# Performance work log

Hardware: AMD Instinct MI355X
Metric: run time of the kernel (lower is better)

## Reference

```python
import jax, jax.numpy as jnp
import numpy as np

WSZ = 8
HEADS = 8
FILTER_RATE = 0.3
EPS = 1e-5


def layer_norm(x, w, b):
    mu = x.mean(-1, keepdims=True)
    var = ((x - mu) ** 2).mean(-1, keepdims=True)
    return (x - mu) * jax.lax.rsqrt(var + EPS) * w + b


def setup_inputs() -> dict:
    key = jax.random.key(0)
    ks = jax.random.split(key, 8)
    B, C, H, W = 2, 256, 512, 512
    C2 = 2 * C
    s = 0.02
    return {
        "feature_map": jax.random.normal(ks[0], (B, C, H, W), jnp.float32),
        "uncertain_map": jax.random.uniform(ks[1], (B, H, W), jnp.float32),
        "norm_w": jnp.ones((C,), jnp.float32),
        "norm_b": jnp.zeros((C,), jnp.float32),
        "lin0_w": jax.random.normal(ks[2], (C, C2), jnp.float32) * s,
        "lin0_b": jnp.zeros((C2,), jnp.float32),
        "qkv0_w": jax.random.normal(ks[3], (C2, 3 * C2), jnp.float32) * s,
        "lin1_w": jax.random.normal(ks[4], (C2, C2), jnp.float32) * s,
        "lin1_b": jnp.zeros((C2,), jnp.float32),
        "qkv1_w": jax.random.normal(ks[5], (C2, 3 * C2), jnp.float32) * s,
        "proj_w": jax.random.normal(ks[6], (C2, C), jnp.float32) * s,
        "proj_b": jnp.zeros((C,), jnp.float32),
    }


def _window_attn(xf, qkv_w, scale, winsz, C2):
    # xf: (N, winsz, C2)
    qkv = (xf @ qkv_w).reshape(-1, winsz, 3, HEADS, C2 // HEADS)
    q, k, v = qkv[:, :, 0], qkv[:, :, 1], qkv[:, :, 2]  # (N, winsz, H, dh)
    a = jnp.einsum("nqhd,nkhd->nhqk", q, k) * scale
    a = jax.nn.softmax(a, axis=-1)
    o = jnp.einsum("nhqk,nkhd->nqhd", a, v).reshape(-1, winsz, C2)
    return xf + o


def reference(feature_map, uncertain_map, norm_w, norm_b, lin0_w, lin0_b,
              qkv0_w, lin1_w, lin1_b, qkv1_w, proj_w, proj_b):
    B, C, H, W = feature_map.shape
    wsz = WSZ
    nH, nW = H // wsz, W // wsz
    nWin, winsz = nH * nW, wsz * wsz
    nWF = int(nWin * FILTER_RATE)
    C2 = 2 * C
    scale = (C // HEADS) ** -0.5  # module uses C//num_heads, not C2//num_heads

    # window partition
    x = jnp.transpose(feature_map, (0, 2, 3, 1))  # B H W C
    win_x = x.reshape(B, nH, wsz, nW, wsz, C).transpose(0, 1, 3, 2, 4, 5)
    win_x = win_x.reshape(B * nWin, winsz, C)
    win_unc = uncertain_map.reshape(B, nH, wsz, nW, wsz).transpose(0, 1, 3, 2, 4)
    win_unc = win_unc.reshape(B, nWin, winsz)

    # topk window selection by mean uncertainty
    score = win_unc.mean(-1)  # (B, nWin)
    _, idx = jax.lax.top_k(score, nWF)  # (B, nWF)
    flat_idx = (idx + jnp.arange(B)[:, None] * nWin).reshape(-1)  # (B*nWF,)

    xw = win_x[flat_idx]  # gather: (B*nWF, winsz, C)
    xn = layer_norm(xw, norm_w, norm_b)

    # local branch: repeat 0
    xf = jax.nn.gelu(xn @ lin0_w + lin0_b, approximate=False)
    xf = _window_attn(xf, qkv0_w, scale, winsz, C2)
    # repeat 1
    xf = xf + jax.nn.gelu(xf @ lin1_w + lin1_b, approximate=False)
    xf = _window_attn(xf, qkv1_w, scale, winsz, C2)

    out_f = xn + jax.nn.gelu(xf @ proj_w + proj_b, approximate=False)

    # scatter-add back into unnormalized windows
    win_x = win_x.at[flat_idx].add(out_f)

    x = win_x.reshape(B, nH, nW, wsz, wsz, C).transpose(0, 1, 3, 2, 4, 5)
    x = x.reshape(B, H, W, C)
    return jnp.transpose(x, (0, 3, 1, 2))
```

## Files before the change

kernel.cpp:

```cpp
#include <hip/hip_runtime.h>
#include <math.h>

typedef unsigned short u16;
typedef unsigned int   u32;
typedef __attribute__((ext_vector_type(8))) short bf16x8;
typedef __attribute__((ext_vector_type(4))) float f32x4;

#define DEV static __device__ __forceinline__

DEV u16 f2b(float f) {
  union { float f; u32 u; } v; v.f = f;
  u32 r = v.u + 0x7FFFu + ((v.u >> 16) & 1u);
  return (u16)(r >> 16);
}
DEV float b2f(u16 h) {
  union { u32 u; float f; } v; v.u = ((u32)h) << 16;
  return v.f;
}
DEV float gelu_f(float x) { return 0.5f * x * (1.0f + erff(x * 0.70710678118654752f)); }

DEV void gload16(const u16* g, u16* l) {
  __builtin_amdgcn_global_load_lds(
      (const __attribute__((address_space(1))) void*)g,
      (__attribute__((address_space(3))) void*)l, 16, 0, 0);
}

__global__ void k_transpose_w(const float* __restrict__ src, u16* __restrict__ dst,
                              int K, int N) {
  long t = (long)blockIdx.x * 256 + threadIdx.x;
  if (t >= (long)K * N) return;
  int n = (int)(t / K), k = (int)(t % K);
  dst[t] = f2b(src[(long)k * N + n]);
}

__global__ void k_scores(const float* __restrict__ unc, float* __restrict__ scores) {
  int id = blockIdx.x * 256 + threadIdx.x;
  if (id >= 8192) return;
  int b = id >> 12, win = id & 4095;
  int h0 = (win >> 6) << 3, w0 = (win & 63) << 3;
  float r[8] = {0.f,0.f,0.f,0.f,0.f,0.f,0.f,0.f};
  for (int i = 0; i < 8; ++i) {
    long base = ((long)(b * 512 + h0 + i)) * 512 + w0;
    #pragma unroll
    for (int j = 0; j < 8; ++j) r[j] += unc[base + j];
  }
  float s = ((r[0] + r[1]) + (r[2] + r[3])) + ((r[4] + r[5]) + (r[6] + r[7]));
  scores[id] = s * (1.0f / 64.0f);
}

__global__ __launch_bounds__(1024) void k_topk(
    const float* __restrict__ scores, int* __restrict__ row2win,
    int* __restrict__ win2row, int nWF) {
  __shared__ float ls[4096];
  __shared__ int   li[4096];
  const int b = blockIdx.x;
  const int tid = threadIdx.x;
  for (int i = tid; i < 4096; i += 1024) {
    ls[i] = scores[b * 4096 + i];
    li[i] = i;
    win2row[b * 4096 + i] = -1;
  }
  __syncthreads();
  for (int k = 2; k <= 4096; k <<= 1) {
    for (int j = k >> 1; j > 0; j >>= 1) {
      for (int t = tid; t < 2048; t += 1024) {
        int i = ((t / j) * (j << 1)) + (t % j);
        int ixj = i + j;
        bool up = ((i & k) == 0);
        float sa = ls[i], sb = ls[ixj];
        int ia = li[i], ib = li[ixj];
        bool g = (sa > sb) || (sa == sb && ia < ib);
        if (g != up) { ls[i] = sb; ls[ixj] = sa; li[i] = ib; li[ixj] = ia; }
      }
      __syncthreads();
    }
  }
  for (int r = tid; r < nWF; r += 1024) {
    int win = li[r];
    row2win[b * nWF + r] = (b << 12) | win;
    win2row[b * 4096 + win] = b * nWF + r;
  }
}

__global__ __launch_bounds__(256) void k_gather_ln(
    const float* __restrict__ fm, const float* __restrict__ nw,
    const float* __restrict__ nb, const int* __restrict__ row2win,
    u16* __restrict__ xn, int winStart) {
  __shared__ float sx[64 * 256];
  const int tid = threadIdx.x;
  const int rw = row2win[winStart + blockIdx.x];
  const int b = rw >> 12, win = rw & 4095;
  const int h0 = (win >> 6) << 3, w0 = (win & 63) << 3;
  {
    const int c8 = tid >> 3, h = tid & 7;
    #pragma unroll
    for (int cc = 0; cc < 8; ++cc) {
      const int c = cc * 32 + c8;
      long base = ((long)(b * 256 + c) * 512 + h0 + h) * 512 + w0;
      float4 v0 = *(const float4*)(fm + base);
      float4 v1 = *(const float4*)(fm + base + 4);
      float vv[8] = {v0.x, v0.y, v0.z, v0.w, v1.x, v1.y, v1.z, v1.w};
      #pragma unroll
      for (int j = 0; j < 8; ++j) {
        int tok = h * 8 + j;
        sx[tok * 256 + (c ^ ((tok & 15) << 1))] = vv[j];
      }
    }
  }
  __syncthreads();
  const int tok = tid >> 2, g = tid & 3;
  const int swz = (tok & 15) << 1;
  float sum = 0.f;
  for (int q = 0; q < 64; ++q) sum += sx[tok * 256 + ((g * 64 + q) ^ swz)];
  sum += __shfl_xor(sum, 1);
  sum += __shfl_xor(sum, 2);
  const float mu = sum * (1.0f / 256.0f);
  float s2 = 0.f;
  for (int q = 0; q < 64; ++q) {
    float d = sx[tok * 256 + ((g * 64 + q) ^ swz)] - mu;
    s2 += d * d;
  }
  s2 += __shfl_xor(s2, 1);
  s2 += __shfl_xor(s2, 2);
  const float rs = rsqrtf(s2 * (1.0f / 256.0f) + 1e-5f);
  long obase = ((long)blockIdx.x * 64 + tok) * 256 + g * 64;
  for (int q8 = 0; q8 < 8; ++q8) {
    u16 tmp[8];
    #pragma unroll
    for (int e = 0; e < 8; ++e) {
      int c = g * 64 + q8 * 8 + e;
      float v = (sx[tok * 256 + (c ^ swz)] - mu) * rs * nw[c] + nb[c];
      tmp[e] = f2b(v);
    }
    *(ulonglong2*)(xn + obase + q8 * 8) = *(const ulonglong2*)tmp;
  }
}

template <int EPI, int NT, int KD>
__global__ __launch_bounds__(512, 2) void k_gemm256(
    const u16* __restrict__ A, const u16* __restrict__ Bt,
    const float* __restrict__ bias, const u16* __restrict__ Res,
    u16* __restrict__ Y, int N, int nWork) {
  constexpr int NKT = KD / 64;
  constexpr int LG_NKT = (KD == 512) ? 3 : 2;
  constexpr int NIP = KD / 128;
  constexpr int LG_NIP = (KD == 512) ? 2 : 1;
  __shared__ __attribute__((aligned(16))) u16 S[65536];
  const int tid = threadIdx.x;
  const int l = tid & 63, wid = tid >> 6;
  const int wm = wid >> 2, wn = wid & 3;

  const int slot = ((blockIdx.x & 7) << 5) | (blockIdx.x >> 3);
  const int q = nWork >> 8, rr = nWork & 255;
  const int wrkBase = slot * q + (slot < rr ? slot : rr);
  const int myN = q + (slot < rr ? 1 : 0);
  if (myN == 0) return;

  const int srow = wid * 8 + (l >> 3);
  const int k0b = ((l & 7) << 4) ^ ((l >> 3) << 4);
  const int vko = k0b >> 1;
  char* ldsS = (char*)S + wid * 1024 + l * 16;
  const char* Sb = (const char*)S;

  f32x4 acc[8][4] = {};
  bf16x8 bfrag[4][2];
  bf16x8 af[2][2];

#define STG(G, ISB, H) do { \
    const int wig_ = (G) >> LG_NKT; \
    const int ktg_ = (G) & (NKT - 1); \
    const int wrkg_ = wrkBase + wig_; \
    const int tmg_ = wrkg_ / NT, tng_ = wrkg_ % NT; \
    const u16* g_ = (ISB) ? Bt + (long)(tng_ * 256 + srow) * KD + vko \
                          : A + (long)(tmg_ * 256 + srow) * KD + vko; \
    char* lp_ = ldsS + ((G) & 1) * 65536 + (ISB) * 32768 + (H) * 16384; \
    gload16(g_ + (long)((H) * 128) * KD + ktg_ * 64, (u16*)lp_); \
    gload16(g_ + (long)((H) * 128 + 64) * KD + ktg_ * 64, (u16*)(lp_ + 8192)); \
  } while (0)

#define DS_B(T) do { \
    _Pragma("unroll") for (int ni_ = 0; ni_ < 4; ++ni_) { \
      const int r_ = wn * 64 + ni_ * 16 + (l & 15); \
      _Pragma("unroll") for (int kk_ = 0; kk_ < 2; ++kk_) { \
        const int kb_ = kk_ * 64 + ((l >> 4) << 4); \
        bfrag[ni_][kk_] = *(const bf16x8*)(Sb + ((T) & 1) * 65536 + 32768 + r_ * 128 + (kb_ ^ ((r_ & 7) << 4))); \
      } } \
  } while (0)

#define DS_A(T, Q) do { \
    _Pragma("unroll") for (int m2_ = 0; m2_ < 2; ++m2_) { \
      const int r_ = wm * 128 + (2 * (Q) + m2_) * 16 + (l & 15); \
      _Pragma("unroll") for (int kk_ = 0; kk_ < 2; ++kk_) { \
        const int kb_ = kk_ * 64 + ((l >> 4) << 4); \
        af[m2_][kk_] = *(const bf16x8*)(Sb + ((T) & 1) * 65536 + r_ * 128 + (kb_ ^ ((r_ & 7) << 4))); \
      } } \
  } while (0)

#define MFMA16(Q) do { \
    _Pragma("unroll") for (int m2_ = 0; m2_ < 2; ++m2_) \
      _Pragma("unroll") for (int ni_ = 0; ni_ < 4; ++ni_) \
        _Pragma("unroll") for (int kk_ = 0; kk_ < 2; ++kk_) \
          acc[2 * (Q) + m2_][ni_] = __builtin_amdgcn_mfma_f32_16x16x32_bf16( \
              af[m2_][kk_], bfrag[ni_][kk_], acc[2 * (Q) + m2_][ni_], 0, 0, 0); \
  } while (0)

#define BAR_MFMA(Q) do { \
    __builtin_amdgcn_s_barrier(); \
    asm volatile("s_waitcnt lgkmcnt(0)" ::: "memory"); \
    __builtin_amdgcn_sched_barrier(0); \
    __builtin_amdgcn_s_setprio(1); \
    MFMA16(Q); \
    __builtin_amdgcn_s_setprio(0); \
  } while (0)

#define PH_END() do { \
    __builtin_amdgcn_s_barrier(); \
    __builtin_amdgcn_sched_barrier(0); \
  } while (0)

  STG(0, 0, 0); STG(0, 0, 1); STG(0, 1, 0); STG(0, 1, 1);
  STG(1, 0, 0); STG(1, 0, 1); STG(1, 1, 0); STG(1, 1, 1);
  asm volatile("s_waitcnt vmcnt(8)" ::: "memory");
  __builtin_amdgcn_s_barrier();
  __builtin_amdgcn_sched_barrier(0);

  const int giEnd = myN * NIP;
  for (int gi = 0; gi < giEnd; ++gi) {
    const int t0 = 2 * gi, t1 = t0 + 1;
    const bool more = (gi + 1 < giEnd);
    DS_B(t0); DS_A(t0, 0);
    if (gi > 0) STG(t1, 0, 0);
    BAR_MFMA(0); PH_END();
    DS_A(t0, 1);
    if (gi > 0) STG(t1, 0, 1);
    if (more) STG(t0 + 2, 1, 0);
    BAR_MFMA(1); PH_END();
    DS_A(t0, 2);
    if (more) STG(t0 + 2, 1, 1);
    BAR_MFMA(2); PH_END();
    DS_A(t0, 3);
    BAR_MFMA(3);
    if (more) { asm volatile("s_waitcnt vmcnt(4)" ::: "memory"); }
    else      { asm volatile("s_waitcnt vmcnt(0)" ::: "memory"); }
    PH_END();
    DS_B(t1); DS_A(t1, 0);
    if (more) STG(t0 + 2, 0, 0);
    BAR_MFMA(0); PH_END();
    DS_A(t1, 1);
    if (more) STG(t0 + 2, 0, 1);
    BAR_MFMA(1); PH_END();
    DS_A(t1, 2);
    if (more) STG(t1 + 2, 1, 0);
    BAR_MFMA(2); PH_END();
    DS_A(t1, 3);
    if (more) STG(t1 + 2, 1, 1);
    BAR_MFMA(3);
    if (more) { asm volatile("s_waitcnt vmcnt(4)" ::: "memory"); }
    PH_END();

    if (((gi + 1) & (NIP - 1)) == 0) {
      const int wrk = wrkBase + (gi >> LG_NIP);
      const int tm = wrk / NT, tn = wrk % NT;
      float bv[4];
      if (EPI >= 1) {
        #pragma unroll
        for (int ni = 0; ni < 4; ++ni)
          bv[ni] = bias[tn * 256 + wn * 64 + ni * 16 + (l & 15)];
      }
      const long rbase = (long)tm * 256 + wm * 128 + ((l >> 4) << 2);
      const int cbase = tn * 256 + wn * 64 + (l & 15);
      #pragma unroll
      for (int mi = 0; mi < 8; ++mi) {
        #pragma unroll
        for (int r = 0; r < 4; ++r) {
          long m = rbase + mi * 16 + r;
          #pragma unroll
          for (int ni = 0; ni < 4; ++ni) {
            int n = cbase + ni * 16;
            float v = acc[mi][ni][r];
            if (EPI >= 1) v = gelu_f(v + bv[ni]);
            if (EPI >= 2) v += b2f(Res[m * N + n]);
            if (EPI == 3) {
              Y[((m >> 6) * 256 + n) * 64 + (m & 63)] = f2b(v);
            } else {
              Y[m * N + n] = f2b(v);
            }
          }
        }
      }
      #pragma unroll
      for (int mi = 0; mi < 8; ++mi)
        #pragma unroll
        for (int ni = 0; ni < 4; ++ni)
          acc[mi][ni] = (f32x4){0.f, 0.f, 0.f, 0.f};
    }
  }
#undef STG
#undef DS_B
#undef DS_A
#undef MFMA16
#undef BAR_MFMA
#undef PH_END
}

__global__ __launch_bounds__(256) void k_attn(
    const u16* __restrict__ qkv, u16* __restrict__ xf) {
  __shared__ __attribute__((aligned(16))) u16 sq[64 * 64];
  __shared__ __attribute__((aligned(16))) u16 sk[64 * 64];
  __shared__ __attribute__((aligned(16))) u16 sv[64 * 64];
  __shared__ __attribute__((aligned(16))) u16 sp[64 * 64];
  const int tid = threadIdx.x;
  const int l = tid & 63, w = tid >> 6;
  const int wloc = blockIdx.x >> 3, h = blockIdx.x & 7;
  const long tokbase = (long)wloc * 64;

  #pragma unroll
  for (int cc = 0; cc < 2; ++cc) {
    int cid = tid * 2 + cc;
    int t = cid >> 3, d0 = (cid & 7) << 3;
    long gq = (tokbase + t) * 1536 + h * 64 + d0;
    ulonglong2 vq = *(const ulonglong2*)(qkv + gq);
    ulonglong2 vk = *(const ulonglong2*)(qkv + gq + 512);
    int sbyte = t * 128 + ((d0 * 2) ^ ((t & 7) << 4));
    *(ulonglong2*)((char*)sq + sbyte) = vq;
    *(ulonglong2*)((char*)sk + sbyte) = vk;
    u16 vv[8];
    *(ulonglong2*)vv = *(const ulonglong2*)(qkv + gq + 1024);
    #pragma unroll
    for (int e = 0; e < 8; ++e) {
      int r = d0 + e;
      *(u16*)((char*)sv + r * 128 + ((t * 2) ^ ((r & 7) << 4))) = vv[e];
    }
  }
  __syncthreads();

  f32x4 accs[4] = {};
  #pragma unroll
  for (int ks = 0; ks < 2; ++ks) {
    int kb = ks * 64 + ((l >> 4) << 4);
    int ra = w * 16 + (l & 15);
    bf16x8 aq = *(const bf16x8*)((char*)sq + ra * 128 + (kb ^ ((ra & 7) << 4)));
    #pragma unroll
    for (int cf = 0; cf < 4; ++cf) {
      int rb = cf * 16 + (l & 15);
      bf16x8 bk = *(const bf16x8*)((char*)sk + rb * 128 + (kb ^ ((rb & 7) << 4)));
      accs[cf] = __builtin_amdgcn_mfma_f32_16x16x32_bf16(aq, bk, accs[cf], 0, 0, 0);
    }
  }
  const float scale = 0.17677669529663687f;
  float pv[4][4];
  #pragma unroll
  for (int r = 0; r < 4; ++r) {
    float m = -1e30f;
    #pragma unroll
    for (int cf = 0; cf < 4; ++cf) {
      pv[cf][r] = accs[cf][r] * scale;
      m = fmaxf(m, pv[cf][r]);
    }
    for (int off = 1; off < 16; off <<= 1) m = fmaxf(m, __shfl_xor(m, off));
    float s = 0.f;
    #pragma unroll
    for (int cf = 0; cf < 4; ++cf) { pv[cf][r] = __expf(pv[cf][r] - m); s += pv[cf][r]; }
    for (int off = 1; off < 16; off <<= 1) s += __shfl_xor(s, off);
    float inv = 1.0f / s;
    #pragma unroll
    for (int cf = 0; cf < 4; ++cf) pv[cf][r] *= inv;
  }
  #pragma unroll
  for (int cf = 0; cf < 4; ++cf)
    #pragma unroll
    for (int r = 0; r < 4; ++r) {
      int pr = w * 16 + ((l >> 4) << 2) + r, pc = cf * 16 + (l & 15);
      *(u16*)((char*)sp + pr * 128 + ((pc * 2) ^ ((pr & 7) << 4))) = f2b(pv[cf][r]);
    }
  __syncthreads();

  f32x4 acco[4] = {};
  #pragma unroll
  for (int ks = 0; ks < 2; ++ks) {
    int kb = ks * 64 + ((l >> 4) << 4);
    int ra = w * 16 + (l & 15);
    bf16x8 ap = *(const bf16x8*)((char*)sp + ra * 128 + (kb ^ ((ra & 7) << 4)));
    #pragma unroll
    for (int cf = 0; cf < 4; ++cf) {
      int rb = cf * 16 + (l & 15);
      bf16x8 bvv = *(const bf16x8*)((char*)sv + rb * 128 + (kb ^ ((rb & 7) << 4)));
      acco[cf] = __builtin_amdgcn_mfma_f32_16x16x32_bf16(ap, bvv, acco[cf], 0, 0, 0);
    }
  }
  #pragma unroll
  for (int cf = 0; cf < 4; ++cf)
    #pragma unroll
    for (int r = 0; r < 4; ++r) {
      long m = tokbase + w * 16 + ((l >> 4) << 2) + r;
      int n = h * 64 + cf * 16 + (l & 15);
      long idx = m * 512 + n;
      xf[idx] = f2b(acco[cf][r] + b2f(xf[idx]));
    }
}

__global__ __launch_bounds__(256) void k_assemble(
    const float* __restrict__ fm, const u16* __restrict__ out_f,
    const int* __restrict__ win2row, float* __restrict__ out) {
  const int tid = threadIdx.x;
  const int bq = blockIdx.x;
  const int hw = bq & 63, c = (bq >> 6) & 255, b = bq >> 14;
  const int w0 = (tid & 127) << 2;
  const int hlo = tid >> 7;
  const int win = hw * 64 + (w0 >> 3);
  const int r = win2row[b * 4096 + win];
  const u16* ofb = out_f + ((long)(r < 0 ? 0 : r) * 256 + c) * 64 + (w0 & 7);
  const long base = ((long)(b * 256 + c) * 512 + hw * 8) * 512 + w0;
  #pragma unroll
  for (int jj = 0; jj < 4; ++jj) {
    const int h = jj * 2 + hlo;
    float4 v = *(const float4*)(fm + base + (long)h * 512);
    if (r >= 0) {
      ushort4 ov = *(const ushort4*)(ofb + h * 8);
      v.x += b2f(ov.x);
      v.y += b2f(ov.y);
      v.z += b2f(ov.z);
      v.w += b2f(ov.w);
    }
    *(float4*)(out + base + (long)h * 512) = v;
  }
}

extern "C" void kernel_launch(void* const* d_in, const int* in_sizes, int n_in,
                              void* d_out, int out_size, void* d_ws, size_t ws_size,
                              hipStream_t stream) {
  const float* fm     = (const float*)d_in[0];
  const float* unc    = (const float*)d_in[1];
  const float* nw     = (const float*)d_in[2];
  const float* nb     = (const float*)d_in[3];
  const float* w_lin0 = (const float*)d_in[4];
  const float* b_lin0 = (const float*)d_in[5];
  const float* w_qkv0 = (const float*)d_in[6];
  const float* w_lin1 = (const float*)d_in[7];
  const float* b_lin1 = (const float*)d_in[8];
  const float* w_qkv1 = (const float*)d_in[9];
  const float* w_proj = (const float*)d_in[10];
  const float* b_proj = (const float*)d_in[11];
  float* out = (float*)d_out;

  const int nWF = 1228, totWin = 2456;
  const long totTok = (long)totWin * 64;

  char* p = (char*)d_ws;
  auto alloc = [&](size_t bytes) {
    char* r = p;
    p += (bytes + 255) & ~(size_t)255;
    return r;
  };
  float* scores = (float*)alloc(8192 * 4);
  int* win2row  = (int*)alloc(8192 * 4);
  int* row2win  = (int*)alloc(totWin * 4);
  u16* wT       = (u16*)alloc((size_t)2097152 * 2);
  u16* out_f    = (u16*)alloc((size_t)(totTok + 256) * 256 * 2);
  size_t persist = (size_t)(p - (char*)d_ws);

  int wpc = totWin;
  {
    const int cands[6] = {1, 2, 4, 8, 16, 32};
    for (int ci = 0; ci < 6; ++ci) {
      int n = cands[ci];
      int wp = ((totWin + n - 1) / n + 3) & ~3;
      size_t mc = (size_t)wp * 64;
      size_t need = persist + 4096 +
                    ((mc * 256 * 2 + 255) & ~(size_t)255) +
                    2 * ((mc * 512 * 2 + 255) & ~(size_t)255) +
                    ((mc * 1536 * 2 + 255) & ~(size_t)255);
      if (need <= ws_size) { wpc = wp; break; }
    }
  }
  long mcap = (long)wpc * 64;
  u16* xn   = (u16*)alloc((size_t)mcap * 256 * 2);
  u16* xfa  = (u16*)alloc((size_t)mcap * 512 * 2);
  u16* xfb  = (u16*)alloc((size_t)mcap * 512 * 2);
  u16* qkvb = (u16*)alloc((size_t)mcap * 1536 * 2);

  u16* wT_lin0 = wT;
  u16* wT_qkv0 = wT + 131072;
  u16* wT_lin1 = wT + 917504;
  u16* wT_qkv1 = wT + 1179648;
  u16* wT_proj = wT + 1966080;
  k_transpose_w<<<(131072 + 255) / 256, 256, 0, stream>>>(w_lin0, wT_lin0, 256, 512);
  k_transpose_w<<<(786432 + 255) / 256, 256, 0, stream>>>(w_qkv0, wT_qkv0, 512, 1536);
  k_transpose_w<<<(262144 + 255) / 256, 256, 0, stream>>>(w_lin1, wT_lin1, 512, 512);
  k_transpose_w<<<(786432 + 255) / 256, 256, 0, stream>>>(w_qkv1, wT_qkv1, 512, 1536);
  k_transpose_w<<<(131072 + 255) / 256, 256, 0, stream>>>(w_proj, wT_proj, 512, 256);

  k_scores<<<32, 256, 0, stream>>>(unc, scores);
  k_topk<<<2, 1024, 0, stream>>>(scores, row2win, win2row, nWF);

  for (int w0 = 0; w0 < totWin; w0 += wpc) {
    int rem = totWin - w0;
    int wn = (wpc < rem) ? wpc : rem;
    int mT = wn / 4;
    k_gather_ln<<<wn, 256, 0, stream>>>(fm, nw, nb, row2win, xn, w0);
    k_gemm256<1, 2, 256><<<256, 512, 0, stream>>>(xn, wT_lin0, b_lin0, nullptr, xfa, 512, mT * 2);
    k_gemm256<0, 6, 512><<<256, 512, 0, stream>>>(xfa, wT_qkv0, nullptr, nullptr, qkvb, 1536, mT * 6);
    k_attn<<<wn * 8, 256, 0, stream>>>(qkvb, xfa);
    k_gemm256<2, 2, 512><<<256, 512, 0, stream>>>(xfa, wT_lin1, b_lin1, xfa, xfb, 512, mT * 2);
    k_gemm256<0, 6, 512><<<256, 512, 0, stream>>>(xfb, wT_qkv1, nullptr, nullptr, qkvb, 1536, mT * 6);
    k_attn<<<wn * 8, 256, 0, stream>>>(qkvb, xfb);
    k_gemm256<3, 1, 512><<<256, 512, 0, stream>>>(xfb, wT_proj, b_proj, xn,
                                                  out_f + (long)w0 * 16384, 256, mT * 1);
  }
  k_assemble<<<32768, 256, 0, stream>>>(fm, out_f, win2row, out);
}
```

Baseline: 2.033 ms.

## Stage GEMM epilogue through LDS for coalesced stores and head-major QKV layout

The GEMM epilogue for the non-proj variants now writes the bf16 accumulator tiles into a swizzled LDS buffer and then emits 16-byte row-contiguous global stores, replacing scattered 2-byte stores. The residual add for the lin1 GEMM moves into this vectorized store phase. A new epilogue mode lays the QKV output out as per-window, per-head contiguous q/k/v blocks, so the attention kernel can load its inputs with fully contiguous 16-byte reads. The cost is an extra 32KB of LDS per block, which may reduce occupancy under launch_bounds(512,2), plus extra barriers in the epilogue.

```diff
diff --git a/kernel.cpp b/kernel.cpp
--- a/kernel.cpp
+++ b/kernel.cpp
@@ -146,6 +146,7 @@
   constexpr int NIP = KD / 128;
   constexpr int LG_NIP = (KD == 512) ? 2 : 1;
   __shared__ __attribute__((aligned(16))) u16 S[65536];
+  __shared__ __attribute__((aligned(16))) u16 E[16384];
   const int tid = threadIdx.x;
   const int l = tid & 63, wid = tid >> 6;
   const int wm = wid >> 2, wn = wid & 3;
@@ -261,30 +262,79 @@
     if (((gi + 1) & (NIP - 1)) == 0) {
       const int wrk = wrkBase + (gi >> LG_NIP);
       const int tm = wrk / NT, tn = wrk % NT;
-      float bv[4];
-      if (EPI >= 1) {
+      if (EPI == 3) {
+        float bv[4];
         #pragma unroll
         for (int ni = 0; ni < 4; ++ni)
           bv[ni] = bias[tn * 256 + wn * 64 + ni * 16 + (l & 15)];
-      }
-      const long rbase = (long)tm * 256 + wm * 128 + ((l >> 4) << 2);
-      const int cbase = tn * 256 + wn * 64 + (l & 15);
-      #pragma unroll
-      for (int mi = 0; mi < 8; ++mi) {
+        const long rbase = (long)tm * 256 + wm * 128 + ((l >> 4) << 2);
+        const int cbase = tn * 256 + wn * 64 + (l & 15);
         #pragma unroll
-        for (int r = 0; r < 4; ++r) {
-          long m = rbase + mi * 16 + r;
+        for (int mi = 0; mi < 8; ++mi) {
           #pragma unroll
-          for (int ni = 0; ni < 4; ++ni) {
-            int n = cbase + ni * 16;
-            float v = acc[mi][ni][r];
-            if (EPI >= 1) v = gelu_f(v + bv[ni]);
-            if (EPI >= 2) v += b2f(Res[m * N + n]);
-            if (EPI == 3) {
+          for (int r = 0; r < 4; ++r) {
+            long m = rbase + mi * 16 + r;
+            #pragma unroll
+            for (int ni = 0; ni < 4; ++ni) {
+              int n = cbase + ni * 16;
+              float v = gelu_f(acc[mi][ni][r] + bv[ni]);
+              v += b2f(Res[m * N + n]);
               Y[((m >> 6) * 256 + n) * 64 + (m & 63)] = f2b(v);
+            }
+          }
+        }
+      } else {
+        float bv[4];
+        if (EPI == 1 || EPI == 2) {
+          #pragma unroll
+          for (int ni = 0; ni < 4; ++ni)
+            bv[ni] = bias[tn * 256 + wn * 64 + ni * 16 + (l & 15)];
+        }
+        #pragma unroll
+        for (int sw = 0; sw < 4; ++sw) {
+          #pragma unroll
+          for (int mi2 = 0; mi2 < 2; ++mi2) {
+            const int mi = 2 * sw + mi2;
+            const int lr0 = wm * 32 + mi2 * 16 + ((l >> 4) << 2);
+            #pragma unroll
+            for (int r = 0; r < 4; ++r) {
+              const int lrr = lr0 + r;
+              #pragma unroll
+              for (int ni = 0; ni < 4; ++ni) {
+                float v = acc[mi][ni][r];
+                if (EPI == 1 || EPI == 2) v = gelu_f(v + bv[ni]);
+                const int col = wn * 64 + ni * 16 + (l & 15);
+                E[lrr * 256 + ((((col >> 3) ^ (lrr & 7)) << 3) | (col & 7))] = f2b(v);
+              }
+            }
+          }
+          asm volatile("s_waitcnt lgkmcnt(0)" ::: "memory");
+          __builtin_amdgcn_s_barrier();
+          const int lr2 = tid >> 3;
+          const long m = (long)tm * 256 + (lr2 >> 5) * 128 + sw * 32 + (lr2 & 31);
+          #pragma unroll
+          for (int rd = 0; rd < 4; ++rd) {
+            const int chunk = rd * 8 + (tid & 7);
+            ulonglong2 val = *(const ulonglong2*)(E + lr2 * 256 + ((chunk ^ (lr2 & 7)) << 3));
+            const int n = tn * 256 + chunk * 8;
+            if (EPI == 2) {
+              u16 tv[8], rv[8];
+              *(ulonglong2*)tv = val;
+              *(ulonglong2*)rv = *(const ulonglong2*)(Res + m * N + n);
+              #pragma unroll
+              for (int e = 0; e < 8; ++e) tv[e] = f2b(b2f(tv[e]) + b2f(rv[e]));
+              val = *(const ulonglong2*)tv;
+            }
+            if (EPI == 4) {
+              const long win = m >> 6;
+              const int t_ = n >> 9, h_ = (n >> 6) & 7, d0 = n & 63;
+              *(ulonglong2*)(Y + ((((win * 8 + h_) * 3 + t_) * 64 + (m & 63)) * 64 + d0)) = val;
             } else {
-              Y[m * N + n] = f2b(v);
+              *(ulonglong2*)(Y + m * N + n) = val;
             }
+          }
+          if (sw < 3) {
+            __builtin_amdgcn_s_barrier();
           }
         }
       }
@@ -313,23 +363,25 @@
   const int l = tid & 63, w = tid >> 6;
   const int wloc = blockIdx.x >> 3, h = blockIdx.x & 7;
   const long tokbase = (long)wloc * 64;
-
-  #pragma unroll
-  for (int cc = 0; cc < 2; ++cc) {
-    int cid = tid * 2 + cc;
-    int t = cid >> 3, d0 = (cid & 7) << 3;
-    long gq = (tokbase + t) * 1536 + h * 64 + d0;
-    ulonglong2 vq = *(const ulonglong2*)(qkv + gq);
-    ulonglong2 vk = *(const ulonglong2*)(qkv + gq + 512);
-    int sbyte = t * 128 + ((d0 * 2) ^ ((t & 7) << 4));
-    *(ulonglong2*)((char*)sq + sbyte) = vq;
-    *(ulonglong2*)((char*)sk + sbyte) = vk;
-    u16 vv[8];
-    *(ulonglong2*)vv = *(const ulonglong2*)(qkv + gq + 1024);
-    #pragma unroll
-    for (int e = 0; e < 8; ++e) {
-      int r = d0 + e;
-      *(u16*)((char*)sv + r * 128 + ((t * 2) ^ ((r & 7) << 4))) = vv[e];
+  const u16* base = qkv + (long)blockIdx.x * 12288;
+
+  #pragma unroll
+  for (int rd = 0; rd < 6; ++rd) {
+    const int cid = rd * 256 + tid;
+    ulonglong2 v16 = *(const ulonglong2*)(base + (long)cid * 8);
+    const int t = (cid >> 3) & 63, d0 = (cid & 7) << 3;
+    if (rd < 2) {
+      *(ulonglong2*)((char*)sq + t * 128 + ((d0 * 2) ^ ((t & 7) << 4))) = v16;
+    } else if (rd < 4) {
+      *(ulonglong2*)((char*)sk + t * 128 + ((d0 * 2) ^ ((t & 7) << 4))) = v16;
+    } else {
+      u16 vv[8];
+      *(ulonglong2*)vv = v16;
+      #pragma unroll
+      for (int e = 0; e < 8; ++e) {
+        int r = d0 + e;
+        *(u16*)((char*)sv + r * 128 + ((t * 2) ^ ((r & 7) << 4))) = vv[e];
+      }
     }
   }
   __syncthreads();
@@ -499,10 +551,10 @@
     int mT = wn / 4;
     k_gather_ln<<<wn, 256, 0, stream>>>(fm, nw, nb, row2win, xn, w0);
     k_gemm256<1, 2, 256><<<256, 512, 0, stream>>>(xn, wT_lin0, b_lin0, nullptr, xfa, 512, mT * 2);
-    k_gemm256<0, 6, 512><<<256, 512, 0, stream>>>(xfa, wT_qkv0, nullptr, nullptr, qkvb, 1536, mT * 6);
+    k_gemm256<4, 6, 512><<<256, 512, 0, stream>>>(xfa, wT_qkv0, nullptr, nullptr, qkvb, 1536, mT * 6);
     k_attn<<<wn * 8, 256, 0, stream>>>(qkvb, xfa);
     k_gemm256<2, 2, 512><<<256, 512, 0, stream>>>(xfa, wT_lin1, b_lin1, xfa, xfb, 512, mT * 2);
-    k_gemm256<0, 6, 512><<<256, 512, 0, stream>>>(xfb, wT_qkv1, nullptr, nullptr, qkvb, 1536, mT * 6);
+    k_gemm256<4, 6, 512><<<256, 512, 0, stream>>>(xfb, wT_qkv1, nullptr, nullptr, qkvb, 1536, mT * 6);
     k_attn<<<wn * 8, 256, 0, stream>>>(qkvb, xfb);
     k_gemm256<3, 1, 512><<<256, 512, 0, stream>>>(xfb, wT_proj, b_proj, xn,
                                                   out_f + (long)w0 * 16384, 256, mT * 1);
```

New measurement: 1.983 ms. 2.5% less time.
